# Kernel optimization log

Hardware: AMD Instinct MI355X
Metric: run time of the kernel (lower is better)

## Reference

```python
import jax, jax.numpy as jnp
import numpy as np

B, H, W, C = 32, 64, 64, 512
NH, WH, WW = 16, 8, 8
SH, SW = 4, 4
FF = 2048
META = 384
A = WH * WW
EPS = 1e-5


def _rel_coords_log():
    # pairwise relative coords in log-space, shape (A*A, 2)
    coords = np.stack(np.meshgrid(np.arange(WH), np.arange(WW), indexing='ij')).reshape(2, -1)
    rel = coords[:, :, None] - coords[:, None, :]
    rel = rel.transpose(1, 2, 0).reshape(-1, 2).astype(np.float32)
    return np.sign(rel) * np.log1p(np.abs(rel))


def _attn_mask():
    # shifted-window attention mask, shape (nW, A, A)
    img = np.zeros((H, W), np.float32)
    cnt = 0
    for hs in (slice(0, -WH), slice(-WH, -SH), slice(-SH, None)):
        for ws in (slice(0, -WW), slice(-WW, -SW), slice(-SW, None)):
            img[hs, ws] = cnt
            cnt += 1
    mw = img.reshape(H // WH, WH, W // WW, WW).transpose(0, 2, 1, 3).reshape(-1, A)
    diff = mw[:, None, :] - mw[:, :, None]
    return np.where(diff != 0, -100.0, 0.0).astype(np.float32)


def setup_inputs():
    key = jax.random.key(0)
    ks = jax.random.split(key, 8)
    s = 0.02
    return {
        'x': jax.random.normal(ks[0], (B, H * W, C), jnp.float32),
        'qkv_w': jax.random.normal(ks[1], (C, 3 * C), jnp.float32) * s,
        'qkv_b': jnp.zeros((3 * C,), jnp.float32),
        'proj_w': jax.random.normal(ks[2], (C, C), jnp.float32) * s,
        'proj_b': jnp.zeros((C,), jnp.float32),
        'tau': jnp.ones((NH,), jnp.float32),
        'meta_w1': jax.random.normal(ks[3], (2, META), jnp.float32) * s,
        'meta_b1': jnp.zeros((META,), jnp.float32),
        'meta_w2': jax.random.normal(ks[4], (META, NH), jnp.float32) * s,
        'meta_b2': jnp.zeros((NH,), jnp.float32),
        'norm1_g': jnp.ones((C,), jnp.float32),
        'norm1_b': jnp.zeros((C,), jnp.float32),
        'norm2_g': jnp.ones((C,), jnp.float32),
        'norm2_b': jnp.zeros((C,), jnp.float32),
        'mlp_w1': jax.random.normal(ks[5], (C, FF), jnp.float32) * s,
        'mlp_b1': jnp.zeros((FF,), jnp.float32),
        'mlp_w2': jax.random.normal(ks[6], (FF, C), jnp.float32) * s,
        'mlp_b2': jnp.zeros((C,), jnp.float32),
    }


def _layernorm(x, g, b):
    mu = x.mean(-1, keepdims=True)
    var = ((x - mu) ** 2).mean(-1, keepdims=True)
    return (x - mu) * jax.lax.rsqrt(var + EPS) * g + b


def reference(x, qkv_w, qkv_b, proj_w, proj_b, tau, meta_w1, meta_b1, meta_w2, meta_b2,
              norm1_g, norm1_b, norm2_g, norm2_b, mlp_w1, mlp_b1, mlp_w2, mlp_b2):
    rel_log = jnp.asarray(_rel_coords_log())
    mask = jnp.asarray(_attn_mask())                 # (nW, A, A)
    nW = mask.shape[0]
    hd = C // NH

    # relative position bias from meta MLP (dropout inactive at eval)
    bias = jax.nn.relu(rel_log @ meta_w1 + meta_b1) @ meta_w2 + meta_b2  # (A*A, NH)
    bias = bias.T.reshape(NH, A, A)

    # cyclic shift + window partition
    xr = x.reshape(B, H, W, C)
    xr = jnp.roll(xr, (-SH, -SW), axis=(1, 2))
    xw = xr.reshape(B, H // WH, WH, W // WW, WW, C).transpose(0, 1, 3, 2, 4, 5)
    xw = xw.reshape(B * nW, A, C)

    qkv = (xw @ qkv_w + qkv_b).reshape(B * nW, A, 3, NH, hd).transpose(2, 0, 3, 1, 4)
    q, k, v = qkv[0], qkv[1], qkv[2]                 # (B*nW, NH, A, hd)

    qn = jnp.linalg.norm(q, axis=-1, keepdims=True)
    kn = jnp.linalg.norm(k, axis=-1, keepdims=True)
    denom = jnp.clip(qn * kn.transpose(0, 1, 3, 2), 1e-6, None)
    attn = jnp.einsum('wnid,wnjd->wnij', q, k) / denom
    attn = attn / jnp.clip(tau, 0.01, None).reshape(1, NH, 1, 1)
    attn = attn + bias[None]
    attn = attn.reshape(B, nW, NH, A, A) + mask[None, :, None]
    attn = jax.nn.softmax(attn.reshape(B * nW, NH, A, A), axis=-1)

    out = jnp.einsum('wnij,wnjd->wnid', attn, v)
    out = out.transpose(0, 2, 1, 3).reshape(B * nW, A, C)
    out = out @ proj_w + proj_b

    # window reverse + reverse shift
    out = out.reshape(B, H // WH, W // WW, WH, WW, C).transpose(0, 1, 3, 2, 4, 5).reshape(B, H, W, C)
    out = jnp.roll(out, (SH, SW), axis=(1, 2)).reshape(B, H * W, C)

    # swin-v2 post-norm residuals
    x = x + _layernorm(out, norm1_g, norm1_b)
    hmid = jax.nn.gelu(x @ mlp_w1 + mlp_b1, approximate=False) @ mlp_w2 + mlp_b2
    x = x + _layernorm(hmid, norm2_g, norm2_b)
    return x
```

## Files before the change

kernel.cpp:

```cpp
#include <hip/hip_runtime.h>

typedef unsigned short u16;
typedef __attribute__((ext_vector_type(8))) short     bf16x8;
typedef __attribute__((ext_vector_type(8))) unsigned short u16x8;
typedef __attribute__((ext_vector_type(4))) unsigned short u16x4;
typedef __attribute__((ext_vector_type(4))) float     f32x4;

#define GADDR(p) ((const __attribute__((address_space(1))) void*)(p))
#define LADDR(p) ((__attribute__((address_space(3))) void*)(p))

__device__ __forceinline__ u16 f2bf(float f) {
  unsigned u = __float_as_uint(f);
  u += 0x7fffu + ((u >> 16) & 1u);
  return (u16)(u >> 16);
}
__device__ __forceinline__ float bf2f(u16 h) {
  return __uint_as_float(((unsigned)h) << 16);
}

__global__ void wt_kernel(const float* __restrict__ w, u16* __restrict__ wt,
                          int K, int N) {
  size_t idx = (size_t)blockIdx.x * 256 + threadIdx.x;
  if (idx >= (size_t)K * N) return;
  int n = (int)(idx / K);
  int k = (int)(idx % K);
  wt[idx] = f2bf(w[(size_t)k * N + n]);
}

__global__ __launch_bounds__(64)
void bias_kernel(const float* __restrict__ w1, const float* __restrict__ b1,
                 const float* __restrict__ w2, const float* __restrict__ b2,
                 float* __restrict__ out) {
  const int p = blockIdx.x;
  const int i = p >> 6, j = p & 63;
  const float d0 = (float)((i >> 3) - (j >> 3));
  const float d1 = (float)((i & 7) - (j & 7));
  const float r0 = copysignf(log1pf(fabsf(d0)), d0);
  const float r1 = copysignf(log1pf(fabsf(d1)), d1);
  float part[16];
#pragma unroll
  for (int h = 0; h < 16; ++h) part[h] = 0.f;
  for (int m = threadIdx.x; m < 384; m += 64) {
    float hv = fmaxf(r0 * w1[m] + r1 * w1[384 + m] + b1[m], 0.f);
#pragma unroll
    for (int h = 0; h < 16; ++h) part[h] += hv * w2[m * 16 + h];
  }
#pragma unroll
  for (int h = 0; h < 16; ++h) {
    float v = part[h];
#pragma unroll
    for (int off = 32; off; off >>= 1) v += __shfl_xor(v, off);
    if (threadIdx.x == 0) out[(size_t)h * 4096 + p] = v + b2[h];
  }
}

__global__ __launch_bounds__(64)
void bias2_kernel(const float* __restrict__ bb, float* __restrict__ b2) {
  const int blk = blockIdx.x;
  const int h = blk >> 4, mi = (blk >> 2) & 3, ni = blk & 3;
  const int lane = threadIdx.x, fr = lane & 15, fq = lane >> 4;
  float4 o;
  o.x = bb[(size_t)h * 4096 + (mi * 16 + fq * 4 + 0) * 64 + ni * 16 + fr];
  o.y = bb[(size_t)h * 4096 + (mi * 16 + fq * 4 + 1) * 64 + ni * 16 + fr];
  o.z = bb[(size_t)h * 4096 + (mi * 16 + fq * 4 + 2) * 64 + ni * 16 + fr];
  o.w = bb[(size_t)h * 4096 + (mi * 16 + fq * 4 + 3) * 64 + ni * 16 + fr];
  ((float4*)b2)[(size_t)blk * 64 + lane] = o;
}

__global__ __launch_bounds__(128)
void partition_kernel(const float* __restrict__ x, u16* __restrict__ xw) {
  const size_t r = blockIdx.x;
  const int w   = (int)(r >> 6);
  const int i   = (int)(r & 63);
  const int b   = w >> 6;
  const int win = w & 63;
  const int hs = (((win >> 3) << 3) + (i >> 3) + 4) & 63;
  const int ws2 = (((win & 7) << 3) + (i & 7) + 4) & 63;
  const float4* src = (const float4*)(x + (((size_t)b << 12) + hs * 64 + ws2) * 512);
  u16* dst = xw + r * 512;
  const int t = threadIdx.x;
  float4 v = src[t];
  u16x4 o;
  o[0] = f2bf(v.x); o[1] = f2bf(v.y); o[2] = f2bf(v.z); o[3] = f2bf(v.w);
  *(u16x4*)(dst + t * 4) = o;
}

template <int MODE>
__global__ __launch_bounds__(512, 2)
void gemm8(const u16* __restrict__ A, const u16* __restrict__ Wt,
           const float* __restrict__ bias, void* __restrict__ outp,
           int M, int N, int K) {
  __shared__ u16 lds[4 * 16384];
  const int t = threadIdx.x;
  const int gx = gridDim.x;
  const int nwg = gx * gridDim.y;
  const int wg = blockIdx.y * gx + blockIdx.x;
  const int swz = (wg & 7) * (nwg >> 3) + (wg >> 3);
  const int n0 = (swz % gx) * 256;
  const int m0 = (swz / gx) * 256;

  const int lane = t & 63;
  const int wid = t >> 6;
  const int wr = (wid >> 2) * 128;
  const int wc = (wid & 3) * 64;
  const int fr = lane & 15, fq = lane >> 4;
  const int rx = (fr >> 1) & 3;

  const int srow = t >> 2;
  const int schk = ((t & 3) ^ ((srow >> 1) & 3)) * 8;
  const u16* Ag0 = A  + (size_t)(m0 + srow) * K + schk;
  const u16* Ag1 = Ag0 + (size_t)128 * K;
  const u16* Bg0 = Wt + (size_t)(n0 + srow) * K + schk;
  const u16* Bg1 = Bg0 + (size_t)128 * K;

#define STAGE_A(tile) do {                                                    \
    const int _o = ((tile) & 3) * 16384 + t * 8;                              \
    const size_t _k = (size_t)(tile) * 32;                                    \
    __builtin_amdgcn_global_load_lds(GADDR(Ag0 + _k), LADDR(&lds[_o]), 16, 0, 0); \
    __builtin_amdgcn_global_load_lds(GADDR(Ag1 + _k), LADDR(&lds[_o + 4096]), 16, 0, 0); \
  } while (0)
#define STAGE_B(tile) do {                                                    \
    const int _o = ((tile) & 3) * 16384 + t * 8;                              \
    const size_t _k = (size_t)(tile) * 32;                                    \
    __builtin_amdgcn_global_load_lds(GADDR(Bg0 + _k), LADDR(&lds[_o + 8192]), 16, 0, 0); \
    __builtin_amdgcn_global_load_lds(GADDR(Bg1 + _k), LADDR(&lds[_o + 12288]), 16, 0, 0); \
  } while (0)

  f32x4 acc[8][4];
#pragma unroll
  for (int a = 0; a < 8; ++a)
#pragma unroll
    for (int b = 0; b < 4; ++b) acc[a][b] = (f32x4){0.f, 0.f, 0.f, 0.f};

  const int NT = K >> 5;
  STAGE_A(0); STAGE_B(0); STAGE_A(1); STAGE_B(1); STAGE_A(2); STAGE_B(2);

  for (int u = 0; u < NT; ++u) {
    if (u + 2 < NT)      asm volatile("s_waitcnt vmcnt(8)" ::: "memory");
    else if (u + 1 < NT) asm volatile("s_waitcnt vmcnt(4)" ::: "memory");
    else                 asm volatile("s_waitcnt vmcnt(0)" ::: "memory");
    __builtin_amdgcn_s_barrier();

    const u16* lb = lds + (u & 3) * 16384;
    bf16x8 bfr[4], af0[4], af1[4];
#pragma unroll
    for (int ni = 0; ni < 4; ++ni)
      bfr[ni] = *(const bf16x8*)&lb[8192 + (wc + ni * 16 + fr) * 32 + (fq ^ rx) * 8];
#pragma unroll
    for (int mi = 0; mi < 4; ++mi)
      af0[mi] = *(const bf16x8*)&lb[(wr + mi * 16 + fr) * 32 + (fq ^ rx) * 8];
    if (u + 3 < NT) STAGE_A(u + 3);
#pragma unroll
    for (int mi = 0; mi < 4; ++mi)
      af1[mi] = *(const bf16x8*)&lb[(wr + 64 + mi * 16 + fr) * 32 + (fq ^ rx) * 8];
    if (u + 3 < NT) STAGE_B(u + 3);

    __builtin_amdgcn_s_setprio(1);
#pragma unroll
    for (int mi = 0; mi < 4; ++mi)
#pragma unroll
      for (int ni = 0; ni < 4; ++ni)
        acc[mi][ni] = __builtin_amdgcn_mfma_f32_16x16x32_bf16(
            af0[mi], bfr[ni], acc[mi][ni], 0, 0, 0);
    __builtin_amdgcn_s_setprio(0);
    __builtin_amdgcn_s_setprio(1);
#pragma unroll
    for (int mi = 0; mi < 4; ++mi)
#pragma unroll
      for (int ni = 0; ni < 4; ++ni)
        acc[4 + mi][ni] = __builtin_amdgcn_mfma_f32_16x16x32_bf16(
            af1[mi], bfr[ni], acc[4 + mi][ni], 0, 0, 0);
    __builtin_amdgcn_s_setprio(0);
  }
#undef STAGE_A
#undef STAGE_B

  __syncthreads();
  float bv4[4];
#pragma unroll
  for (int ni = 0; ni < 4; ++ni) bv4[ni] = bias[n0 + wc + ni * 16 + fr];

  u16* uW = &lds[wid * 8192];
  u16* og = (u16*)outp;
#pragma unroll
  for (int mi = 0; mi < 8; ++mi) {
#pragma unroll
    for (int ni = 0; ni < 4; ++ni)
#pragma unroll
      for (int j = 0; j < 4; ++j) {
        float v = acc[mi][ni][j] + bv4[ni];
        if (MODE == 2) {
          const float a2 = v * (1.5957691216f + 0.0713548162f * v * v);
          const float e = __expf(a2);
          v = v * (e * __builtin_amdgcn_rcpf(e + 1.0f));
        }
        uW[(fq * 4 + j) * 64 + ((ni ^ j ^ fq) & 3) * 16 + fr] = f2bf(v);
      }
#pragma unroll
    for (int p = 0; p < 2; ++p) {
      const int r = p * 8 + (lane >> 3);
      const int sg = (((lane & 7) >> 1) ^ (r & 3) ^ ((r >> 2) & 3)) & 3;
      u16x8 v8 = *(const u16x8*)&uW[r * 64 + sg * 16 + (lane & 1) * 8];
      const int row = m0 + wr + mi * 16 + r;
      *(u16x8*)&og[(size_t)row * N + n0 + wc + (lane & 7) * 8] = v8;
    }
  }
}

template <int LNM>
__global__ __launch_bounds__(512, 1)
void gemm_ln(const u16* __restrict__ A, const u16* __restrict__ Wt,
             const float* __restrict__ bias, const float* __restrict__ resid,
             const float* __restrict__ g, const float* __restrict__ bt,
             float* __restrict__ out1, u16* __restrict__ out1b, int K) {
  __shared__ u16 lds[61440];
  const int t = threadIdx.x;
  const int nwg = gridDim.x;
  const int wg = blockIdx.x;
  const int swz = (wg & 7) * (nwg >> 3) + (wg >> 3);
  const int m0 = swz * 128;

  const int lane = t & 63;
  const int wid = t >> 6;
  const int wc = wid * 64;
  const int fr = lane & 15, fq = lane >> 4;
  const int rx = (fr >> 1) & 3;

  const int srow = t >> 2;
  const int schk = ((t & 3) ^ ((srow >> 1) & 3)) * 8;
  const u16* Ag = A  + (size_t)(m0 + srow) * K + schk;
  const u16* Bg = Wt + (size_t)srow * K + schk;

#define GLSTAGE_A(tile, buf)                                                  \
    __builtin_amdgcn_global_load_lds(GADDR(Ag + (size_t)(tile) * 32),         \
        LADDR(&lds[(buf) * 20480 + t * 8]), 16, 0, 0)
#define GLSTAGE_B(tile, buf, p)                                               \
    __builtin_amdgcn_global_load_lds(                                         \
        GADDR(Bg + (size_t)(p) * 128 * K + (size_t)(tile) * 32),              \
        LADDR(&lds[(buf) * 20480 + 4096 + (p) * 4096 + t * 8]), 16, 0, 0)

  f32x4 acc[8][4];
#pragma unroll
  for (int a = 0; a < 8; ++a)
#pragma unroll
    for (int b = 0; b < 4; ++b) acc[a][b] = (f32x4){0.f, 0.f, 0.f, 0.f};

  const int NT = K >> 5;
  GLSTAGE_A(0, 0);
  GLSTAGE_B(0, 0, 0); GLSTAGE_B(0, 0, 1); GLSTAGE_B(0, 0, 2); GLSTAGE_B(0, 0, 3);
  GLSTAGE_A(1, 1);
  GLSTAGE_B(1, 1, 0); GLSTAGE_B(1, 1, 1); GLSTAGE_B(1, 1, 2); GLSTAGE_B(1, 1, 3);

  int cur = 0;
  for (int u = 0; u < NT; ++u) {
    if (u + 1 < NT) asm volatile("s_waitcnt vmcnt(5)" ::: "memory");
    else            asm volatile("s_waitcnt vmcnt(0)" ::: "memory");
    __builtin_amdgcn_s_barrier();

    const u16* lb = lds + cur * 20480;
    const int stg = (cur == 0) ? 2 : cur - 1;
    bf16x8 bfr[4], af0[4], af1[4];
#pragma unroll
    for (int ni = 0; ni < 4; ++ni)
      bfr[ni] = *(const bf16x8*)&lb[4096 + (wc + ni * 16 + fr) * 32 + (fq ^ rx) * 8];
#pragma unroll
    for (int mi = 0; mi < 4; ++mi)
      af0[mi] = *(const bf16x8*)&lb[(mi * 16 + fr) * 32 + (fq ^ rx) * 8];
    if (u + 2 < NT) {
      GLSTAGE_A(u + 2, stg);
      GLSTAGE_B(u + 2, stg, 0); GLSTAGE_B(u + 2, stg, 1);
    }
#pragma unroll
    for (int mi = 0; mi < 4; ++mi)
      af1[mi] = *(const bf16x8*)&lb[((4 + mi) * 16 + fr) * 32 + (fq ^ rx) * 8];
    if (u + 2 < NT) {
      GLSTAGE_B(u + 2, stg, 2); GLSTAGE_B(u + 2, stg, 3);
    }

    __builtin_amdgcn_s_setprio(1);
#pragma unroll
    for (int mi = 0; mi < 4; ++mi)
#pragma unroll
      for (int ni = 0; ni < 4; ++ni)
        acc[mi][ni] = __builtin_amdgcn_mfma_f32_16x16x32_bf16(
            af0[mi], bfr[ni], acc[mi][ni], 0, 0, 0);
    __builtin_amdgcn_s_setprio(0);
    __builtin_amdgcn_s_setprio(1);
#pragma unroll
    for (int mi = 0; mi < 4; ++mi)
#pragma unroll
      for (int ni = 0; ni < 4; ++ni)
        acc[4 + mi][ni] = __builtin_amdgcn_mfma_f32_16x16x32_bf16(
            af1[mi], bfr[ni], acc[4 + mi][ni], 0, 0, 0);
    __builtin_amdgcn_s_setprio(0);
    cur = (cur == 2) ? 0 : cur + 1;
  }
#undef GLSTAGE_A
#undef GLSTAGE_B

  __syncthreads();
  float bv4[4];
#pragma unroll
  for (int ni = 0; ni < 4; ++ni) bv4[ni] = bias[wc + ni * 16 + fr];
  float4 ga = ((const float4*)g)[lane * 2];
  float4 gb = ((const float4*)g)[lane * 2 + 1];
  float4 ba = ((const float4*)bt)[lane * 2];
  float4 bb = ((const float4*)bt)[lane * 2 + 1];
  const float gv[8] = {ga.x, ga.y, ga.z, ga.w, gb.x, gb.y, gb.z, gb.w};
  const float bv[8] = {ba.x, ba.y, ba.z, ba.w, bb.x, bb.y, bb.z, bb.w};
  float* fLN = (float*)lds;

#pragma unroll
  for (int mi = 0; mi < 8; ++mi) {
#pragma unroll
    for (int ni = 0; ni < 4; ++ni)
#pragma unroll
      for (int j = 0; j < 4; ++j) {
        const int ch = ((wid * 4 + ni) ^ (j << 2) ^ fq) & 31;
        fLN[(fq * 4 + j) * 512 + ch * 16 + fr] = acc[mi][ni][j] + bv4[ni];
      }
    __syncthreads();
#pragma unroll
    for (int rr = 0; rr < 2; ++rr) {
      const int r = wid * 2 + rr;
      const int gci = lane >> 1;
      const int ch = (gci ^ ((r & 3) << 2) ^ (r >> 2)) & 31;
      const int base = r * 512 + ch * 16 + (lane & 1) * 8;
      f32x4 va = *(const f32x4*)&fLN[base];
      f32x4 vb = *(const f32x4*)&fLN[base + 4];
      float v[8] = {va[0], va[1], va[2], va[3], vb[0], vb[1], vb[2], vb[3]};
      float s = 0.f, s2 = 0.f;
#pragma unroll
      for (int e = 0; e < 8; ++e) { s += v[e]; s2 = fmaf(v[e], v[e], s2); }
#pragma unroll
      for (int off = 32; off; off >>= 1) {
        s += __shfl_xor(s, off); s2 += __shfl_xor(s2, off);
      }
      const float mu = s * (1.f / 512.f);
      const float rs = rsqrtf(s2 * (1.f / 512.f) - mu * mu + 1e-5f);
      const int rowg = m0 + mi * 16 + r;
      size_t token;
      if (LNM == 0) {
        const int w = rowg >> 6, i = rowg & 63;
        const int b = w >> 6, win = w & 63;
        const int hs = (((win >> 3) << 3) + (i >> 3) + 4) & 63;
        const int ws2 = (((win & 7) << 3) + (i & 7) + 4) & 63;
        token = ((size_t)b << 12) + hs * 64 + ws2;
      } else {
        token = (size_t)rowg;
      }
      const float* rp = resid + token * 512 + lane * 8;
      float4 r0 = ((const float4*)rp)[0];
      float4 r1 = ((const float4*)rp)[1];
      const float rv[8] = {r0.x, r0.y, r0.z, r0.w, r1.x, r1.y, r1.z, r1.w};
      float o[8];
      u16x8 ob;
#pragma unroll
      for (int e = 0; e < 8; ++e) {
        o[e] = rv[e] + (v[e] - mu) * rs * gv[e] + bv[e];
        ob[e] = f2bf(o[e]);
      }
      float* op = out1 + token * 512 + lane * 8;
      ((f32x4*)op)[0] = (f32x4){o[0], o[1], o[2], o[3]};
      ((f32x4*)op)[1] = (f32x4){o[4], o[5], o[6], o[7]};
      if (LNM == 0) *(u16x8*)(out1b + token * 512 + lane * 8) = ob;
    }
    __syncthreads();
  }
}

__global__ __launch_bounds__(64)
void attn_kernel(const u16* __restrict__ qkv, const float* __restrict__ bias2,
                 const float* __restrict__ tau, u16* __restrict__ ao) {
  const int h = blockIdx.x;
  const int w = blockIdx.y;
  const int lane = threadIdx.x;
  const int fr = lane & 15, fq = lane >> 4;

  __shared__ u16 sh[7424];

  const size_t rowb = ((size_t)w * 64 + lane) * 1536 + (size_t)h * 32;
  u16x8 q8[4], k8[4], v8[4];
#pragma unroll
  for (int u = 0; u < 4; ++u) {
    q8[u] = ((const u16x8*)(qkv + rowb))[u];
    k8[u] = ((const u16x8*)(qkv + rowb + 512))[u];
    v8[u] = ((const u16x8*)(qkv + rowb + 1024))[u];
  }
  float qv[32], kv[32];
  float qn = 0.f, kn = 0.f;
#pragma unroll
  for (int d = 0; d < 32; ++d) {
    qv[d] = bf2f(q8[d >> 3][d & 7]); qn = fmaf(qv[d], qv[d], qn);
    kv[d] = bf2f(k8[d >> 3][d & 7]); kn = fmaf(kv[d], kv[d], kn);
  }
  const float itau = 1.0f / fmaxf(tau[h], 0.01f);
  const float qs = rsqrtf(fmaxf(qn, 1e-24f)) * itau;
  const float ks = rsqrtf(fmaxf(kn, 1e-24f));
#pragma unroll
  for (int u = 0; u < 4; ++u) {
    u16x8 qo, ko;
#pragma unroll
    for (int e = 0; e < 8; ++e) {
      qo[e] = f2bf(qv[u * 8 + e] * qs);
      ko[e] = f2bf(kv[u * 8 + e] * ks);
    }
    *(u16x8*)&sh[lane * 40 + u * 8] = qo;
    *(u16x8*)&sh[2560 + lane * 40 + u * 8] = ko;
  }
#pragma unroll
  for (int d = 0; d < 32; ++d)
    sh[5120 + d * 72 + lane] = v8[d >> 3][d & 7];
  __syncthreads();

  f32x4 acc[4][4];
  const float4* b2 = (const float4*)bias2 + (size_t)h * 1024 + lane;
#pragma unroll
  for (int mi = 0; mi < 4; ++mi)
#pragma unroll
    for (int ni = 0; ni < 4; ++ni) {
      float4 bv = b2[(mi * 4 + ni) * 64];
      acc[mi][ni] = (f32x4){bv.x, bv.y, bv.z, bv.w};
    }
  const int win = w & 63, wh = win >> 3, ww = win & 7;
  if (wh == 7 || ww == 7) {
    int labc[4];
#pragma unroll
    for (int ni = 0; ni < 4; ++ni) {
      const int c = ni * 16 + fr;
      labc[ni] = ((wh == 7) ? (((c >> 3) < 4) ? 1 : 2) : 0) * 3
               + ((ww == 7) ? (((c & 7) < 4) ? 1 : 2) : 0);
    }
#pragma unroll
    for (int mi = 0; mi < 4; ++mi)
#pragma unroll
      for (int j = 0; j < 4; ++j) {
        const int r = mi * 16 + fq * 4 + j;
        const int lr = ((wh == 7) ? (((r >> 3) < 4) ? 1 : 2) : 0) * 3
                     + ((ww == 7) ? (((r & 7) < 4) ? 1 : 2) : 0);
#pragma unroll
        for (int ni = 0; ni < 4; ++ni)
          if (lr != labc[ni]) acc[mi][ni][j] -= 100.f;
      }
  }

  {
    bf16x8 af[4], bf[4];
#pragma unroll
    for (int mi = 0; mi < 4; ++mi)
      af[mi] = *(const bf16x8*)&sh[(mi * 16 + fr) * 40 + fq * 8];
#pragma unroll
    for (int ni = 0; ni < 4; ++ni)
      bf[ni] = *(const bf16x8*)&sh[2560 + (ni * 16 + fr) * 40 + fq * 8];
#pragma unroll
    for (int mi = 0; mi < 4; ++mi)
#pragma unroll
      for (int ni = 0; ni < 4; ++ni)
        acc[mi][ni] = __builtin_amdgcn_mfma_f32_16x16x32_bf16(
            af[mi], bf[ni], acc[mi][ni], 0, 0, 0);
  }

  float lrec[4][4];
#pragma unroll
  for (int mi = 0; mi < 4; ++mi) {
#pragma unroll
    for (int j = 0; j < 4; ++j) {
      float m4 = fmaxf(fmaxf(acc[mi][0][j], acc[mi][1][j]),
                       fmaxf(acc[mi][2][j], acc[mi][3][j]));
#pragma unroll
      for (int mk = 1; mk < 16; mk <<= 1) m4 = fmaxf(m4, __shfl_xor(m4, mk));
      float e0 = __expf(acc[mi][0][j] - m4);
      float e1 = __expf(acc[mi][1][j] - m4);
      float e2 = __expf(acc[mi][2][j] - m4);
      float e3 = __expf(acc[mi][3][j] - m4);
      float s4 = (e0 + e1) + (e2 + e3);
#pragma unroll
      for (int mk = 1; mk < 16; mk <<= 1) s4 += __shfl_xor(s4, mk);
      lrec[mi][j] = __builtin_amdgcn_rcpf(s4);
      const int r = mi * 16 + fq * 4 + j;
      sh[r * 72 +  0 + fr] = f2bf(e0);
      sh[r * 72 + 16 + fr] = f2bf(e1);
      sh[r * 72 + 32 + fr] = f2bf(e2);
      sh[r * 72 + 48 + fr] = f2bf(e3);
    }
  }
  __syncthreads();

  f32x4 acc2[4][2];
#pragma unroll
  for (int mi = 0; mi < 4; ++mi)
#pragma unroll
    for (int n2 = 0; n2 < 2; ++n2) acc2[mi][n2] = (f32x4){0.f, 0.f, 0.f, 0.f};
#pragma unroll
  for (int kk = 0; kk < 2; ++kk) {
    bf16x8 pf[4], vf[2];
#pragma unroll
    for (int mi = 0; mi < 4; ++mi)
      pf[mi] = *(const bf16x8*)&sh[(mi * 16 + fr) * 72 + kk * 32 + fq * 8];
#pragma unroll
    for (int n2 = 0; n2 < 2; ++n2)
      vf[n2] = *(const bf16x8*)&sh[5120 + (n2 * 16 + fr) * 72 + kk * 32 + fq * 8];
#pragma unroll
    for (int mi = 0; mi < 4; ++mi)
#pragma unroll
      for (int n2 = 0; n2 < 2; ++n2)
        acc2[mi][n2] = __builtin_amdgcn_mfma_f32_16x16x32_bf16(
            pf[mi], vf[n2], acc2[mi][n2], 0, 0, 0);
  }

  u16* op = ao + ((size_t)w * 64) * 512 + (size_t)h * 32;
#pragma unroll
  for (int mi = 0; mi < 4; ++mi)
#pragma unroll
    for (int j = 0; j < 4; ++j) {
      const int r = mi * 16 + fq * 4 + j;
      const float sc = lrec[mi][j];
      op[(size_t)r * 512 +  0 + fr] = f2bf(acc2[mi][0][j] * sc);
      op[(size_t)r * 512 + 16 + fr] = f2bf(acc2[mi][1][j] * sc);
    }
}

extern "C" void kernel_launch(void* const* d_in, const int* in_sizes, int n_in,
                              void* d_out, int out_size, void* d_ws, size_t ws_size,
                              hipStream_t stream) {
  const float* x      = (const float*)d_in[0];
  const float* qkv_w  = (const float*)d_in[1];
  const float* qkv_b  = (const float*)d_in[2];
  const float* proj_w = (const float*)d_in[3];
  const float* proj_b = (const float*)d_in[4];
  const float* tau    = (const float*)d_in[5];
  const float* mw1    = (const float*)d_in[6];
  const float* mb1    = (const float*)d_in[7];
  const float* mw2    = (const float*)d_in[8];
  const float* mb2    = (const float*)d_in[9];
  const float* n1g    = (const float*)d_in[10];
  const float* n1b    = (const float*)d_in[11];
  const float* n2g    = (const float*)d_in[12];
  const float* n2b    = (const float*)d_in[13];
  const float* mlp_w1 = (const float*)d_in[14];
  const float* mlp_b1 = (const float*)d_in[15];
  const float* mlp_w2 = (const float*)d_in[16];
  const float* mlp_b2 = (const float*)d_in[17];

  char* ws = (char*)d_ws;
  u16*   WQKVT  = (u16*)  (ws + 0);
  u16*   WPROJT = (u16*)  (ws + 1572864);
  u16*   WM1T   = (u16*)  (ws + 2097152);
  u16*   WM2T   = (u16*)  (ws + 4194304);
  float* BIASB  = (float*)(ws + 6291456);
  float* BIAS2  = (float*)(ws + 6553600);
  const size_t CH0 = 8388608;

  int CB = 32;
  while (CB > 1 && CH0 + (size_t)CB * 33554432ull > ws_size) CB >>= 1;
  const int NCH = 32 / CB;
  const size_t Mc = (size_t)CB * 4096;

  u16*   XW   = (u16*)  (ws + CH0);
  u16*   QKV  = (u16*)  (ws + CH0 + Mc * 1024);
  u16*   HBUF = QKV;
  float* X1   = (float*)(ws + CH0 + Mc * 5120);
  u16*   X1B  = (u16*)  (ws + CH0 + Mc * 7168);
  u16*   AO   = XW;

  wt_kernel<<<(512 * 1536 + 255) / 256, 256, 0, stream>>>(qkv_w, WQKVT, 512, 1536);
  wt_kernel<<<(512 * 512 + 255) / 256, 256, 0, stream>>>(proj_w, WPROJT, 512, 512);
  wt_kernel<<<(512 * 2048 + 255) / 256, 256, 0, stream>>>(mlp_w1, WM1T, 512, 2048);
  wt_kernel<<<(2048 * 512 + 255) / 256, 256, 0, stream>>>(mlp_w2, WM2T, 2048, 512);
  bias_kernel<<<4096, 64, 0, stream>>>(mw1, mb1, mw2, mb2, BIASB);
  bias2_kernel<<<256, 64, 0, stream>>>(BIASB, BIAS2);

  const unsigned MB = (unsigned)(Mc / 256);
  const unsigned LB = (unsigned)(Mc / 128);

  for (int c = 0; c < NCH; ++c) {
    const float* xc = x + (size_t)c * Mc * 512;
    float* oc = (float*)d_out + (size_t)c * Mc * 512;

    partition_kernel<<<(unsigned)Mc, 128, 0, stream>>>(xc, XW);
    gemm8<0><<<dim3(6, MB), 512, 0, stream>>>(XW, WQKVT, qkv_b, QKV,
                                              (int)Mc, 1536, 512);
    attn_kernel<<<dim3(16, CB * 64), 64, 0, stream>>>(QKV, BIAS2, tau, AO);
    gemm_ln<0><<<LB, 512, 0, stream>>>(AO, WPROJT, proj_b, xc, n1g, n1b,
                                       X1, X1B, 512);
    gemm8<2><<<dim3(8, MB), 512, 0, stream>>>(X1B, WM1T, mlp_b1, HBUF,
                                              (int)Mc, 2048, 512);
    gemm_ln<1><<<LB, 512, 0, stream>>>(HBUF, WM2T, mlp_b2, X1, n2g, n2b,
                                       oc, nullptr, 2048);
  }
}
```

Before: 1.532 ms.

## Restructure GEMM main loop into 64-wide K tiles with interleaved quadrant staging

Reworks the bf16 GEMM mainloop to use a K-tile of 64 with double buffering instead of a 4-deep ring of 32-wide tiles. Each iteration is split into four MFMA quadrants, with barriers between them, and the global-to-LDS loads for future tiles are interleaved between those phases in a ping-pong style schedule. The LDS swizzle is changed to an XOR over 8 chunks to match the wider rows, and occupancy drops to one workgroup per CU. The intent is better overlap of memory and MFMA work with fewer waits per K, at the cost of many more barriers and lower occupancy.

```diff
diff --git a/kernel.cpp b/kernel.cpp
--- a/kernel.cpp
+++ b/kernel.cpp
@@ -86,44 +86,48 @@
 }
 
 template <int MODE>
-__global__ __launch_bounds__(512, 2)
+__global__ __launch_bounds__(512, 1)
 void gemm8(const u16* __restrict__ A, const u16* __restrict__ Wt,
            const float* __restrict__ bias, void* __restrict__ outp,
            int M, int N, int K) {
-  __shared__ u16 lds[4 * 16384];
+  __shared__ u16 lds[65536];
   const int t = threadIdx.x;
   const int gx = gridDim.x;
   const int nwg = gx * gridDim.y;
   const int wg = blockIdx.y * gx + blockIdx.x;
-  const int swz = (wg & 7) * (nwg >> 3) + (wg >> 3);
-  const int n0 = (swz % gx) * 256;
-  const int m0 = (swz / gx) * 256;
+  const int swzb = (wg & 7) * (nwg >> 3) + (wg >> 3);
+  const int n0 = (swzb % gx) * 256;
+  const int m0 = (swzb / gx) * 256;
 
   const int lane = t & 63;
   const int wid = t >> 6;
   const int wr = (wid >> 2) * 128;
   const int wc = (wid & 3) * 64;
   const int fr = lane & 15, fq = lane >> 4;
-  const int rx = (fr >> 1) & 3;
-
-  const int srow = t >> 2;
-  const int schk = ((t & 3) ^ ((srow >> 1) & 3)) * 8;
-  const u16* Ag0 = A  + (size_t)(m0 + srow) * K + schk;
-  const u16* Ag1 = Ag0 + (size_t)128 * K;
-  const u16* Bg0 = Wt + (size_t)(n0 + srow) * K + schk;
-  const u16* Bg1 = Bg0 + (size_t)128 * K;
-
-#define STAGE_A(tile) do {                                                    \
-    const int _o = ((tile) & 3) * 16384 + t * 8;                              \
-    const size_t _k = (size_t)(tile) * 32;                                    \
-    __builtin_amdgcn_global_load_lds(GADDR(Ag0 + _k), LADDR(&lds[_o]), 16, 0, 0); \
-    __builtin_amdgcn_global_load_lds(GADDR(Ag1 + _k), LADDR(&lds[_o + 4096]), 16, 0, 0); \
+  const int c0 = (fq ^ (fr & 7)) * 8;
+  const int c1 = ((4 + fq) ^ (fr & 7)) * 8;
+
+  const int tq = t >> 3;
+  const int scol = ((t & 7) ^ (tq & 7)) * 8;
+  const u16* Asrc = A  + (size_t)(m0 + tq) * K + scol;
+  const int rowB = (tq & 31) + ((t >> 8) << 6);
+  const u16* Bsrc = Wt + (size_t)(n0 + rowB) * K + scol;
+  const int dA = t * 8;
+  const int dB = 16384 + ((t >> 8) << 11) + t * 8;
+
+#define SG_A(tile, src, h) do {                                               \
+    const int _d = ((tile) & 1) * 32768 + (h) * 4096 + dA;                    \
+    const size_t _k = (size_t)(src) * 64 + (size_t)((h) * 64) * K;            \
+    __builtin_amdgcn_global_load_lds(GADDR(Asrc + _k), LADDR(&lds[_d]), 16, 0, 0); \
+    __builtin_amdgcn_global_load_lds(GADDR(Asrc + _k + (size_t)128 * K),      \
+                                     LADDR(&lds[_d + 8192]), 16, 0, 0);       \
   } while (0)
-#define STAGE_B(tile) do {                                                    \
-    const int _o = ((tile) & 3) * 16384 + t * 8;                              \
-    const size_t _k = (size_t)(tile) * 32;                                    \
-    __builtin_amdgcn_global_load_lds(GADDR(Bg0 + _k), LADDR(&lds[_o + 8192]), 16, 0, 0); \
-    __builtin_amdgcn_global_load_lds(GADDR(Bg1 + _k), LADDR(&lds[_o + 12288]), 16, 0, 0); \
+#define SG_B(tile, src, h) do {                                               \
+    const int _d = ((tile) & 1) * 32768 + (h) * 2048 + dB;                    \
+    const size_t _k = (size_t)(src) * 64 + (size_t)((h) * 32) * K;            \
+    __builtin_amdgcn_global_load_lds(GADDR(Bsrc + _k), LADDR(&lds[_d]), 16, 0, 0); \
+    __builtin_amdgcn_global_load_lds(GADDR(Bsrc + _k + (size_t)128 * K),      \
+                                     LADDR(&lds[_d + 8192]), 16, 0, 0);       \
   } while (0)
 
   f32x4 acc[8][4];
@@ -132,50 +136,111 @@
 #pragma unroll
     for (int b = 0; b < 4; ++b) acc[a][b] = (f32x4){0.f, 0.f, 0.f, 0.f};
 
-  const int NT = K >> 5;
-  STAGE_A(0); STAGE_B(0); STAGE_A(1); STAGE_B(1); STAGE_A(2); STAGE_B(2);
-
-  for (int u = 0; u < NT; ++u) {
-    if (u + 2 < NT)      asm volatile("s_waitcnt vmcnt(8)" ::: "memory");
-    else if (u + 1 < NT) asm volatile("s_waitcnt vmcnt(4)" ::: "memory");
-    else                 asm volatile("s_waitcnt vmcnt(0)" ::: "memory");
-    __builtin_amdgcn_s_barrier();
-
-    const u16* lb = lds + (u & 3) * 16384;
-    bf16x8 bfr[4], af0[4], af1[4];
-#pragma unroll
-    for (int ni = 0; ni < 4; ++ni)
-      bfr[ni] = *(const bf16x8*)&lb[8192 + (wc + ni * 16 + fr) * 32 + (fq ^ rx) * 8];
-#pragma unroll
-    for (int mi = 0; mi < 4; ++mi)
-      af0[mi] = *(const bf16x8*)&lb[(wr + mi * 16 + fr) * 32 + (fq ^ rx) * 8];
-    if (u + 3 < NT) STAGE_A(u + 3);
-#pragma unroll
-    for (int mi = 0; mi < 4; ++mi)
-      af1[mi] = *(const bf16x8*)&lb[(wr + 64 + mi * 16 + fr) * 32 + (fq ^ rx) * 8];
-    if (u + 3 < NT) STAGE_B(u + 3);
-
+  const int NT = K >> 6;
+  SG_A(0, 0, 0); SG_A(0, 0, 1); SG_B(0, 0, 0); SG_B(0, 0, 1);
+  SG_A(1, 1, 0); SG_B(1, 1, 0); SG_B(1, 1, 1);
+  asm volatile("s_waitcnt vmcnt(6)" ::: "memory");
+  __builtin_amdgcn_s_barrier();
+
+  for (int s = 0; s < NT; ++s) {
+    const int sb = (s & 1) << 15;
+    const u16* la = lds + sb;
+    const u16* lb = lds + sb + 16384;
+    bf16x8 af[8], bf0[4], bf1[4];
+#pragma unroll
+    for (int mi = 0; mi < 4; ++mi) {
+      const int r = (wr + mi * 16 + fr) * 64;
+      af[mi * 2]     = *(const bf16x8*)&la[r + c0];
+      af[mi * 2 + 1] = *(const bf16x8*)&la[r + c1];
+    }
+#pragma unroll
+    for (int ni = 0; ni < 2; ++ni) {
+      const int r = (wc + ni * 16 + fr) * 64;
+      bf0[ni * 2]     = *(const bf16x8*)&lb[r + c0];
+      bf0[ni * 2 + 1] = *(const bf16x8*)&lb[r + c1];
+    }
+    if (s + 1 < NT) SG_A(s + 1, s + 1, 1);
+    __builtin_amdgcn_s_barrier();
+    asm volatile("s_waitcnt lgkmcnt(0)" ::: "memory");
+    __builtin_amdgcn_sched_barrier(0);
     __builtin_amdgcn_s_setprio(1);
 #pragma unroll
     for (int mi = 0; mi < 4; ++mi)
 #pragma unroll
-      for (int ni = 0; ni < 4; ++ni)
+      for (int ni = 0; ni < 2; ++ni) {
         acc[mi][ni] = __builtin_amdgcn_mfma_f32_16x16x32_bf16(
-            af0[mi], bfr[ni], acc[mi][ni], 0, 0, 0);
+            af[mi * 2], bf0[ni * 2], acc[mi][ni], 0, 0, 0);
+        acc[mi][ni] = __builtin_amdgcn_mfma_f32_16x16x32_bf16(
+            af[mi * 2 + 1], bf0[ni * 2 + 1], acc[mi][ni], 0, 0, 0);
+      }
     __builtin_amdgcn_s_setprio(0);
+    __builtin_amdgcn_s_barrier();
+#pragma unroll
+    for (int ni = 0; ni < 2; ++ni) {
+      const int r = (wc + 32 + ni * 16 + fr) * 64;
+      bf1[ni * 2]     = *(const bf16x8*)&lb[r + c0];
+      bf1[ni * 2 + 1] = *(const bf16x8*)&lb[r + c1];
+    }
+    if (s + 2 < NT) SG_A(s + 2, s + 2, 0);
+    __builtin_amdgcn_s_barrier();
+    asm volatile("s_waitcnt lgkmcnt(0)" ::: "memory");
+    __builtin_amdgcn_sched_barrier(0);
     __builtin_amdgcn_s_setprio(1);
 #pragma unroll
     for (int mi = 0; mi < 4; ++mi)
 #pragma unroll
-      for (int ni = 0; ni < 4; ++ni)
+      for (int ni = 0; ni < 2; ++ni) {
+        acc[mi][2 + ni] = __builtin_amdgcn_mfma_f32_16x16x32_bf16(
+            af[mi * 2], bf1[ni * 2], acc[mi][2 + ni], 0, 0, 0);
+        acc[mi][2 + ni] = __builtin_amdgcn_mfma_f32_16x16x32_bf16(
+            af[mi * 2 + 1], bf1[ni * 2 + 1], acc[mi][2 + ni], 0, 0, 0);
+      }
+    __builtin_amdgcn_s_setprio(0);
+    __builtin_amdgcn_s_barrier();
+#pragma unroll
+    for (int mi = 0; mi < 4; ++mi) {
+      const int r = (wr + 64 + mi * 16 + fr) * 64;
+      af[mi * 2]     = *(const bf16x8*)&la[r + c0];
+      af[mi * 2 + 1] = *(const bf16x8*)&la[r + c1];
+    }
+    if (s + 2 < NT) SG_B(s + 2, s + 2, 0);
+    __builtin_amdgcn_s_barrier();
+    asm volatile("s_waitcnt lgkmcnt(0)" ::: "memory");
+    __builtin_amdgcn_sched_barrier(0);
+    __builtin_amdgcn_s_setprio(1);
+#pragma unroll
+    for (int mi = 0; mi < 4; ++mi)
+#pragma unroll
+      for (int ni = 0; ni < 2; ++ni) {
         acc[4 + mi][ni] = __builtin_amdgcn_mfma_f32_16x16x32_bf16(
-            af1[mi], bfr[ni], acc[4 + mi][ni], 0, 0, 0);
+            af[mi * 2], bf0[ni * 2], acc[4 + mi][ni], 0, 0, 0);
+        acc[4 + mi][ni] = __builtin_amdgcn_mfma_f32_16x16x32_bf16(
+            af[mi * 2 + 1], bf0[ni * 2 + 1], acc[4 + mi][ni], 0, 0, 0);
+      }
     __builtin_amdgcn_s_setprio(0);
-  }
-#undef STAGE_A
-#undef STAGE_B
-
+    __builtin_amdgcn_s_barrier();
+    if (s + 2 < NT) SG_B(s + 2, s + 2, 1);
+    __builtin_amdgcn_s_barrier();
+    __builtin_amdgcn_s_setprio(1);
+#pragma unroll
+    for (int mi = 0; mi < 4; ++mi)
+#pragma unroll
+      for (int ni = 0; ni < 2; ++ni) {
+        acc[4 + mi][2 + ni] = __builtin_amdgcn_mfma_f32_16x16x32_bf16(
+            af[mi * 2], bf1[ni * 2], acc[4 + mi][2 + ni], 0, 0, 0);
+        acc[4 + mi][2 + ni] = __builtin_amdgcn_mfma_f32_16x16x32_bf16(
+            af[mi * 2 + 1], bf1[ni * 2 + 1], acc[4 + mi][2 + ni], 0, 0, 0);
+      }
+    __builtin_amdgcn_s_setprio(0);
+    if (s + 2 < NT) asm volatile("s_waitcnt vmcnt(6)" ::: "memory");
+    else            asm volatile("s_waitcnt vmcnt(0)" ::: "memory");
+    __builtin_amdgcn_s_barrier();
+  }
+#undef SG_A
+#undef SG_B
+  asm volatile("s_waitcnt vmcnt(0)" ::: "memory");
   __syncthreads();
+
   float bv4[4];
 #pragma unroll
   for (int ni = 0; ni < 4; ++ni) bv4[ni] = bias[n0 + wc + ni * 16 + fr];
```

After: 1.503 ms. No clear change (-1.9%).

## Restructure GEMM main loop into 8-wave ping-pong with BK=64 double buffering

Applied to the files above, without the earlier changes.

Rewrites the bf16 GEMM mainloop to use K-tiles of 64 with two LDS slots, a new XOR swizzle for 64-wide rows, and a four-phase schedule per tile. Each phase interleaves partial global-to-LDS staging with MFMA quadrants, separated by barriers and priority raises, in the style of an HipKittens-like 8-wave ping-pong. Launch bounds drop to one block per CU. The aim is better overlap of loads with MFMA and fewer LDS reads per K element, at the cost of many more barriers and lower occupancy.

```diff
diff --git a/kernel.cpp b/kernel.cpp
--- a/kernel.cpp
+++ b/kernel.cpp
@@ -86,44 +86,48 @@
 }
 
 template <int MODE>
-__global__ __launch_bounds__(512, 2)
+__global__ __launch_bounds__(512, 1)
 void gemm8(const u16* __restrict__ A, const u16* __restrict__ Wt,
            const float* __restrict__ bias, void* __restrict__ outp,
            int M, int N, int K) {
-  __shared__ u16 lds[4 * 16384];
+  __shared__ u16 lds[65536];
   const int t = threadIdx.x;
   const int gx = gridDim.x;
   const int nwg = gx * gridDim.y;
   const int wg = blockIdx.y * gx + blockIdx.x;
-  const int swz = (wg & 7) * (nwg >> 3) + (wg >> 3);
-  const int n0 = (swz % gx) * 256;
-  const int m0 = (swz / gx) * 256;
+  const int swzb = (wg & 7) * (nwg >> 3) + (wg >> 3);
+  const int n0 = (swzb % gx) * 256;
+  const int m0 = (swzb / gx) * 256;
 
   const int lane = t & 63;
   const int wid = t >> 6;
   const int wr = (wid >> 2) * 128;
   const int wc = (wid & 3) * 64;
   const int fr = lane & 15, fq = lane >> 4;
-  const int rx = (fr >> 1) & 3;
-
-  const int srow = t >> 2;
-  const int schk = ((t & 3) ^ ((srow >> 1) & 3)) * 8;
-  const u16* Ag0 = A  + (size_t)(m0 + srow) * K + schk;
-  const u16* Ag1 = Ag0 + (size_t)128 * K;
-  const u16* Bg0 = Wt + (size_t)(n0 + srow) * K + schk;
-  const u16* Bg1 = Bg0 + (size_t)128 * K;
-
-#define STAGE_A(tile) do {                                                    \
-    const int _o = ((tile) & 3) * 16384 + t * 8;                              \
-    const size_t _k = (size_t)(tile) * 32;                                    \
-    __builtin_amdgcn_global_load_lds(GADDR(Ag0 + _k), LADDR(&lds[_o]), 16, 0, 0); \
-    __builtin_amdgcn_global_load_lds(GADDR(Ag1 + _k), LADDR(&lds[_o + 4096]), 16, 0, 0); \
+  const int c0 = (fq ^ (fr & 7)) * 8;
+  const int c1 = ((4 + fq) ^ (fr & 7)) * 8;
+
+  const int tq = t >> 3;
+  const int scol = ((t & 7) ^ (tq & 7)) * 8;
+  const u16* Asrc = A  + (size_t)(m0 + tq) * K + scol;
+  const int rowB = (tq & 31) + ((t >> 8) << 6);
+  const u16* Bsrc = Wt + (size_t)(n0 + rowB) * K + scol;
+  const int dA = t * 8;
+  const int dB = 16384 + ((t >> 8) << 11) + t * 8;
+
+#define SG_A(slot, src, h) do {                                               \
+    const int _d = (slot) * 32768 + (h) * 4096 + dA;                          \
+    const size_t _k = (size_t)(src) * 64 + (size_t)((h) * 64) * K;            \
+    __builtin_amdgcn_global_load_lds(GADDR(Asrc + _k), LADDR(&lds[_d]), 16, 0, 0); \
+    __builtin_amdgcn_global_load_lds(GADDR(Asrc + _k + (size_t)128 * K),      \
+                                     LADDR(&lds[_d + 8192]), 16, 0, 0);       \
   } while (0)
-#define STAGE_B(tile) do {                                                    \
-    const int _o = ((tile) & 3) * 16384 + t * 8;                              \
-    const size_t _k = (size_t)(tile) * 32;                                    \
-    __builtin_amdgcn_global_load_lds(GADDR(Bg0 + _k), LADDR(&lds[_o + 8192]), 16, 0, 0); \
-    __builtin_amdgcn_global_load_lds(GADDR(Bg1 + _k), LADDR(&lds[_o + 12288]), 16, 0, 0); \
+#define SG_B(slot, src, h) do {                                               \
+    const int _d = (slot) * 32768 + (h) * 2048 + dB;                          \
+    const size_t _k = (size_t)(src) * 64 + (size_t)((h) * 32) * K;            \
+    __builtin_amdgcn_global_load_lds(GADDR(Bsrc + _k), LADDR(&lds[_d]), 16, 0, 0); \
+    __builtin_amdgcn_global_load_lds(GADDR(Bsrc + _k + (size_t)128 * K),      \
+                                     LADDR(&lds[_d + 8192]), 16, 0, 0);       \
   } while (0)
 
   f32x4 acc[8][4];
@@ -132,50 +136,117 @@
 #pragma unroll
     for (int b = 0; b < 4; ++b) acc[a][b] = (f32x4){0.f, 0.f, 0.f, 0.f};
 
-  const int NT = K >> 5;
-  STAGE_A(0); STAGE_B(0); STAGE_A(1); STAGE_B(1); STAGE_A(2); STAGE_B(2);
-
-  for (int u = 0; u < NT; ++u) {
-    if (u + 2 < NT)      asm volatile("s_waitcnt vmcnt(8)" ::: "memory");
-    else if (u + 1 < NT) asm volatile("s_waitcnt vmcnt(4)" ::: "memory");
-    else                 asm volatile("s_waitcnt vmcnt(0)" ::: "memory");
-    __builtin_amdgcn_s_barrier();
-
-    const u16* lb = lds + (u & 3) * 16384;
-    bf16x8 bfr[4], af0[4], af1[4];
-#pragma unroll
-    for (int ni = 0; ni < 4; ++ni)
-      bfr[ni] = *(const bf16x8*)&lb[8192 + (wc + ni * 16 + fr) * 32 + (fq ^ rx) * 8];
-#pragma unroll
-    for (int mi = 0; mi < 4; ++mi)
-      af0[mi] = *(const bf16x8*)&lb[(wr + mi * 16 + fr) * 32 + (fq ^ rx) * 8];
-    if (u + 3 < NT) STAGE_A(u + 3);
-#pragma unroll
-    for (int mi = 0; mi < 4; ++mi)
-      af1[mi] = *(const bf16x8*)&lb[(wr + 64 + mi * 16 + fr) * 32 + (fq ^ rx) * 8];
-    if (u + 3 < NT) STAGE_B(u + 3);
-
-    __builtin_amdgcn_s_setprio(1);
-#pragma unroll
-    for (int mi = 0; mi < 4; ++mi)
-#pragma unroll
-      for (int ni = 0; ni < 4; ++ni)
-        acc[mi][ni] = __builtin_amdgcn_mfma_f32_16x16x32_bf16(
-            af0[mi], bfr[ni], acc[mi][ni], 0, 0, 0);
-    __builtin_amdgcn_s_setprio(0);
-    __builtin_amdgcn_s_setprio(1);
-#pragma unroll
-    for (int mi = 0; mi < 4; ++mi)
-#pragma unroll
-      for (int ni = 0; ni < 4; ++ni)
-        acc[4 + mi][ni] = __builtin_amdgcn_mfma_f32_16x16x32_bf16(
-            af1[mi], bfr[ni], acc[4 + mi][ni], 0, 0, 0);
-    __builtin_amdgcn_s_setprio(0);
-  }
-#undef STAGE_A
-#undef STAGE_B
-
+  const int NT = K >> 6;
+  SG_A(0, 0, 0); SG_A(0, 0, 1); SG_B(0, 0, 0); SG_B(0, 0, 1);
+  SG_A(1, 1, 0); SG_B(1, 1, 0); SG_B(1, 1, 1);
+  asm volatile("s_waitcnt vmcnt(6)" ::: "memory");
+  __builtin_amdgcn_s_barrier();
+
+#define TILE_BODY(S, SLOT, NSLOT, P0_COND)                                    \
+  {                                                                           \
+    const u16* la = lds + (SLOT) * 32768;                                     \
+    const u16* lb = la + 16384;                                               \
+    bf16x8 af[8], bf0[4], bf1[4];                                             \
+    _Pragma("unroll")                                                         \
+    for (int mi = 0; mi < 4; ++mi) {                                          \
+      const int r = (wr + mi * 16 + fr) * 64;                                 \
+      af[mi * 2]     = *(const bf16x8*)&la[r + c0];                           \
+      af[mi * 2 + 1] = *(const bf16x8*)&la[r + c1];                           \
+    }                                                                         \
+    _Pragma("unroll")                                                         \
+    for (int ni = 0; ni < 2; ++ni) {                                          \
+      const int r = (wc + ni * 16 + fr) * 64;                                 \
+      bf0[ni * 2]     = *(const bf16x8*)&lb[r + c0];                          \
+      bf0[ni * 2 + 1] = *(const bf16x8*)&lb[r + c1];                          \
+    }                                                                         \
+    if (P0_COND) SG_A(NSLOT, (S) + 1, 1);                                     \
+    __builtin_amdgcn_s_barrier();                                             \
+    asm volatile("s_waitcnt lgkmcnt(0)" ::: "memory");                        \
+    __builtin_amdgcn_sched_barrier(0);                                        \
+    __builtin_amdgcn_s_setprio(1);                                            \
+    _Pragma("unroll")                                                         \
+    for (int mi = 0; mi < 4; ++mi)                                            \
+      _Pragma("unroll")                                                       \
+      for (int ni = 0; ni < 2; ++ni) {                                        \
+        acc[mi][ni] = __builtin_amdgcn_mfma_f32_16x16x32_bf16(                \
+            af[mi * 2], bf0[ni * 2], acc[mi][ni], 0, 0, 0);                   \
+        acc[mi][ni] = __builtin_amdgcn_mfma_f32_16x16x32_bf16(                \
+            af[mi * 2 + 1], bf0[ni * 2 + 1], acc[mi][ni], 0, 0, 0);           \
+      }                                                                       \
+    __builtin_amdgcn_s_setprio(0);                                            \
+    __builtin_amdgcn_s_barrier();                                             \
+    _Pragma("unroll")                                                         \
+    for (int ni = 0; ni < 2; ++ni) {                                          \
+      const int r = (wc + 32 + ni * 16 + fr) * 64;                            \
+      bf1[ni * 2]     = *(const bf16x8*)&lb[r + c0];                          \
+      bf1[ni * 2 + 1] = *(const bf16x8*)&lb[r + c1];                          \
+    }                                                                         \
+    if ((S) + 2 < NT) SG_A(SLOT, (S) + 2, 0);                                 \
+    __builtin_amdgcn_s_barrier();                                             \
+    asm volatile("s_waitcnt lgkmcnt(0)" ::: "memory");                        \
+    __builtin_amdgcn_sched_barrier(0);                                        \
+    __builtin_amdgcn_s_setprio(1);                                            \
+    _Pragma("unroll")                                                         \
+    for (int mi = 0; mi < 4; ++mi)                                            \
+      _Pragma("unroll")                                                       \
+      for (int ni = 0; ni < 2; ++ni) {                                        \
+        acc[mi][2 + ni] = __builtin_amdgcn_mfma_f32_16x16x32_bf16(            \
+            af[mi * 2], bf1[ni * 2], acc[mi][2 + ni], 0, 0, 0);               \
+        acc[mi][2 + ni] = __builtin_amdgcn_mfma_f32_16x16x32_bf16(            \
+            af[mi * 2 + 1], bf1[ni * 2 + 1], acc[mi][2 + ni], 0, 0, 0);       \
+      }                                                                       \
+    __builtin_amdgcn_s_setprio(0);                                            \
+    __builtin_amdgcn_s_barrier();                                             \
+    _Pragma("unroll")                                                         \
+    for (int mi = 0; mi < 4; ++mi) {                                          \
+      const int r = (wr + 64 + mi * 16 + fr) * 64;                            \
+      af[mi * 2]     = *(const bf16x8*)&la[r + c0];                           \
+      af[mi * 2 + 1] = *(const bf16x8*)&la[r + c1];                           \
+    }                                                                         \
+    if ((S) + 2 < NT) SG_B(SLOT, (S) + 2, 0);                                 \
+    __builtin_amdgcn_s_barrier();                                             \
+    asm volatile("s_waitcnt lgkmcnt(0)" ::: "memory");                        \
+    __builtin_amdgcn_sched_barrier(0);                                        \
+    __builtin_amdgcn_s_setprio(1);                                            \
+    _Pragma("unroll")                                                         \
+    for (int mi = 0; mi < 4; ++mi)                                            \
+      _Pragma("unroll")                                                       \
+      for (int ni = 0; ni < 2; ++ni) {                                        \
+        acc[4 + mi][ni] = __builtin_amdgcn_mfma_f32_16x16x32_bf16(            \
+            af[mi * 2], bf0[ni * 2], acc[4 + mi][ni], 0, 0, 0);               \
+        acc[4 + mi][ni] = __builtin_amdgcn_mfma_f32_16x16x32_bf16(            \
+            af[mi * 2 + 1], bf0[ni * 2 + 1], acc[4 + mi][ni], 0, 0, 0);       \
+      }                                                                       \
+    __builtin_amdgcn_s_setprio(0);                                            \
+    __builtin_amdgcn_s_barrier();                                             \
+    if ((S) + 2 < NT) SG_B(SLOT, (S) + 2, 1);                                 \
+    __builtin_amdgcn_s_barrier();                                             \
+    __builtin_amdgcn_s_setprio(1);                                            \
+    _Pragma("unroll")                                                         \
+    for (int mi = 0; mi < 4; ++mi)                                            \
+      _Pragma("unroll")                                                       \
+      for (int ni = 0; ni < 2; ++ni) {                                        \
+        acc[4 + mi][2 + ni] = __builtin_amdgcn_mfma_f32_16x16x32_bf16(        \
+            af[mi * 2], bf1[ni * 2], acc[4 + mi][2 + ni], 0, 0, 0);           \
+        acc[4 + mi][2 + ni] = __builtin_amdgcn_mfma_f32_16x16x32_bf16(        \
+            af[mi * 2 + 1], bf1[ni * 2 + 1], acc[4 + mi][2 + ni], 0, 0, 0);   \
+      }                                                                       \
+    __builtin_amdgcn_s_setprio(0);                                            \
+    if ((S) + 2 < NT) asm volatile("s_waitcnt vmcnt(6)" ::: "memory");        \
+    else              asm volatile("s_waitcnt vmcnt(0)" ::: "memory");        \
+    __builtin_amdgcn_s_barrier();                                             \
+  }
+
+  for (int s = 0; s < NT; s += 2) {
+    TILE_BODY(s,     0, 1, true);
+    TILE_BODY(s + 1, 1, 0, (s + 2 < NT));
+  }
+#undef TILE_BODY
+#undef SG_A
+#undef SG_B
+  asm volatile("s_waitcnt vmcnt(0)" ::: "memory");
   __syncthreads();
+
   float bv4[4];
 #pragma unroll
   for (int ni = 0; ni < 4; ++ni) bv4[ni] = bias[n0 + wc + ni * 16 + fr];
```

New measurement: 1.495 ms. -2.4%, faster.
